# Kernel tuning notes

Measured on AMD Instinct MI355X. Metric: run time of the kernel, lower is better.

The kernel has to match this reference:

```python
import jax, jax.numpy as jnp
import numpy as np

B, T = 1024, 200
V = 100000   # item_size
H = 256      # hidden_size == embedding_size (GRU consumes embedding directly)
NUM_LAYERS = 2


def _gru_layer(x, w_ih, w_hh):
    """PyTorch GRU layer, bias=False. x: [B,T,in], w_ih: [3H,in], w_hh: [3H,H].
    Gate order in weights is (r, z, n)."""
    h0 = jnp.zeros((x.shape[0], w_hh.shape[1]), x.dtype)
    # Precompute all input projections in one big GEMM: [B,T,3H]
    x_proj = jnp.einsum('bti,gi->btg', x, w_ih)

    def step(h, xp):
        hp = h @ w_hh.T                      # [B,3H]
        xr, xz, xn = jnp.split(xp, 3, axis=-1)
        hr, hz, hn = jnp.split(hp, 3, axis=-1)
        r = jax.nn.sigmoid(xr + hr)
        z = jax.nn.sigmoid(xz + hz)
        n = jnp.tanh(xn + r * hn)
        h_new = (1.0 - z) * n + z * h
        return h_new, h_new

    _, ys = jax.lax.scan(step, h0, jnp.swapaxes(x_proj, 0, 1))  # [T,B,H]
    return jnp.swapaxes(ys, 0, 1)  # [B,T,H]


def setup_inputs() -> dict:
    key = jax.random.key(0)
    ks = jax.random.split(key, 8)
    input_ids = jax.random.randint(ks[0], (B, T), 0, V)
    s = 0.05
    emb = jax.random.normal(ks[1], (V, H), jnp.float32) * s
    emb = emb.at[0].set(0.0)  # padding_idx=0
    w_ih_l0 = jax.random.normal(ks[2], (3 * H, H), jnp.float32) * s
    w_hh_l0 = jax.random.normal(ks[3], (3 * H, H), jnp.float32) * s
    w_ih_l1 = jax.random.normal(ks[4], (3 * H, H), jnp.float32) * s
    w_hh_l1 = jax.random.normal(ks[5], (3 * H, H), jnp.float32) * s
    dense_w = jax.random.normal(ks[6], (H, H), jnp.float32) * s  # Linear(H, E=H)
    dense_b = jax.random.normal(ks[7], (H,), jnp.float32) * s
    return {"input_ids": input_ids, "emb": emb,
            "w_ih_l0": w_ih_l0, "w_hh_l0": w_hh_l0,
            "w_ih_l1": w_ih_l1, "w_hh_l1": w_hh_l1,
            "dense_w": dense_w, "dense_b": dense_b}


def reference(input_ids, emb, w_ih_l0, w_hh_l0, w_ih_l1, w_hh_l1, dense_w, dense_b):
    x = emb[input_ids]                 # [B,T,H] embedding lookup
    # emb_dropout is identity in eval mode
    x = _gru_layer(x, w_ih_l0, w_hh_l0)
    x = _gru_layer(x, w_ih_l1, w_hh_l1)
    return x @ dense_w.T + dense_b     # [B,T,H]
```

## Files before the change

kernel.cpp:

```cpp
#include <hip/hip_runtime.h>

#define T_LEN 200
#define HID   256
#define BATCH 1024
#define G3    768
#define ROWS  16
#define NTHREADS 512
#define WSZ   196608

typedef __bf16  bf16x8 __attribute__((ext_vector_type(8)));
typedef float   f32x4  __attribute__((ext_vector_type(4)));

__device__ __forceinline__ unsigned short f2bf(float f) {
  union { float f; unsigned int u; } c; c.f = f;
  unsigned int u = c.u;
  u += 0x7FFFu + ((u >> 16) & 1u);
  return (unsigned short)(u >> 16);
}
__device__ __forceinline__ float bf2f(unsigned int u16v) {
  union { unsigned int u; float f; } c; c.u = u16v << 16; return c.f;
}
__device__ __forceinline__ float sigm(float x) { return 1.0f / (1.0f + __expf(-x)); }
__device__ __forceinline__ float tanh_f(float x) { return 1.0f - 2.0f / (__expf(2.0f * x) + 1.0f); }

__global__ void convert_weights(const float* __restrict__ a,
                                const float* __restrict__ b,
                                const float* __restrict__ c,
                                const float* __restrict__ d,
                                const float* __restrict__ e,
                                unsigned short* __restrict__ out) {
  int i = blockIdx.x * blockDim.x + threadIdx.x;
  const int total = 4 * WSZ + HID * HID;
  if (i >= total) return;
  float v;
  if      (i < 1 * WSZ) v = a[i];
  else if (i < 2 * WSZ) v = b[i - 1 * WSZ];
  else if (i < 3 * WSZ) v = c[i - 2 * WSZ];
  else if (i < 4 * WSZ) v = d[i - 3 * WSZ];
  else                  v = e[i - 4 * WSZ];
  out[i] = f2bf(v);
}

__device__ __forceinline__ bf16x8 lds_frag(const unsigned short* buf, int row, int k, int lq) {
  int chunk = (k << 2) + lq;
  int idx = row * HID + ((chunk ^ (row & 7)) << 3);
  return *reinterpret_cast<const bf16x8*>(buf + idx);
}
__device__ __forceinline__ bf16x8 gw_frag(const unsigned short* __restrict__ W, int wrow, int kof) {
  return *reinterpret_cast<const bf16x8*>(W + (size_t)wrow * HID + kof);
}
__device__ __forceinline__ uint4 gw_fragu(const unsigned short* __restrict__ W, int wrow, int kof) {
  return *reinterpret_cast<const uint4*>(W + (size_t)wrow * HID + kof);
}
__device__ __forceinline__ bf16x8 as_bf(uint4 u) { return __builtin_bit_cast(bf16x8, u); }
__device__ __forceinline__ uint2 pack4(f32x4 v) {
  uint2 r;
  r.x = (unsigned int)f2bf(v[0]) | ((unsigned int)f2bf(v[1]) << 16);
  r.y = (unsigned int)f2bf(v[2]) | ((unsigned int)f2bf(v[3]) << 16);
  return r;
}


template<int GATHER>
__global__ __launch_bounds__(NTHREADS)
void xp_gemm(const int* __restrict__ ids, const float* __restrict__ emb,
             const unsigned short* __restrict__ hsrc,
             const unsigned short* __restrict__ W,
             unsigned short* __restrict__ xpT)
{
  __shared__ __align__(16) unsigned short As[128 * HID];
  const int tid = threadIdx.x;
  const int w = tid >> 6, lane = tid & 63, lr = lane & 15, lq = lane >> 4;
  const int bt = blockIdx.x & 63;
  const int tt = blockIdx.x >> 6;
  const int r0 = bt * 16, t0 = tt * 8;

  for (int idx = tid; idx < 128 * 32; idx += NTHREADS) {
    int row = idx >> 5, cc = idx & 31;
    int bloc = row & 15, tloc = row >> 4;
    int sidx = row * HID + ((cc ^ (row & 7)) << 3);
    if (GATHER) {
      int rid = ids[(r0 + bloc) * T_LEN + t0 + tloc];
      const f32x4* src = reinterpret_cast<const f32x4*>(emb + (size_t)rid * HID + cc * 8);
      f32x4 v0 = src[0], v1 = src[1];
      uint4 pk;
      pk.x = (unsigned int)f2bf(v0[0]) | ((unsigned int)f2bf(v0[1]) << 16);
      pk.y = (unsigned int)f2bf(v0[2]) | ((unsigned int)f2bf(v0[3]) << 16);
      pk.z = (unsigned int)f2bf(v1[0]) | ((unsigned int)f2bf(v1[1]) << 16);
      pk.w = (unsigned int)f2bf(v1[2]) | ((unsigned int)f2bf(v1[3]) << 16);
      *reinterpret_cast<uint4*>(&As[sidx]) = pk;
    } else {
      const unsigned short* hs = hsrc + ((size_t)(t0 + tloc) * 64 + bt) * (ROWS * HID);
      uint4 v = *reinterpret_cast<const uint4*>(hs + bloc * HID + ((cc ^ (bloc & 7)) << 3));
      *reinterpret_cast<uint4*>(&As[sidx]) = v;
    }
  }
  __syncthreads();

  const int colbase = w * 96;
  #pragma unroll 1
  for (int mt = 0; mt < 8; ++mt) {
    bf16x8 a[8];
    #pragma unroll
    for (int k = 0; k < 8; ++k) a[k] = lds_frag(As, mt * 16 + lr, k, lq);
    const int t = t0 + mt;
    unsigned short* xprow = xpT + ((size_t)t * 64 + bt) * (G3 * 16);
    #pragma unroll
    for (int np = 0; np < 3; ++np) {
      const int c0 = colbase + np * 32;
      f32x4 acc0 = {0,0,0,0}, acc1 = {0,0,0,0};
      #pragma unroll
      for (int k = 0; k < 8; ++k) {
        const int kof = k * 32 + lq * 8;
        bf16x8 b0 = gw_frag(W, c0 + lr,      kof);
        bf16x8 b1 = gw_frag(W, c0 + 16 + lr, kof);
        acc0 = __builtin_amdgcn_mfma_f32_16x16x32_bf16(a[k], b0, acc0, 0, 0, 0);
        acc1 = __builtin_amdgcn_mfma_f32_16x16x32_bf16(a[k], b1, acc1, 0, 0, 0);
      }
      *reinterpret_cast<uint2*>(xprow + (c0 + lr)      * 16 + lq * 4) = pack4(acc0);
      *reinterpret_cast<uint2*>(xprow + (c0 + 16 + lr) * 16 + lq * 4) = pack4(acc1);
    }
  }
}

__global__ __launch_bounds__(NTHREADS, 2)
void gru_rec(const unsigned short* __restrict__ xpT,
             const unsigned short* __restrict__ Whh,
             unsigned short* __restrict__ hout)
{
  __shared__ __align__(16) unsigned short hb[2][ROWS * HID];
  const int tid = threadIdx.x;
  const int w = tid >> 6, lane = tid & 63, lr = lane & 15, lq = lane >> 4;
  const int bt = blockIdx.x;
  const int c0 = w * 32;

  uint4 wf[2][3][8];
  #pragma unroll
  for (int j = 0; j < 2; ++j)
    #pragma unroll
    for (int g = 0; g < 3; ++g)
      #pragma unroll
      for (int k = 0; k < 8; ++k)
        wf[j][g][k] = gw_fragu(Whh, g * 256 + c0 + j * 16 + lr, k * 32 + lq * 8);
  #pragma unroll
  for (int j = 0; j < 2; ++j)
    #pragma unroll
    for (int g = 0; g < 3; ++g)
      #pragma unroll
      for (int k = 0; k < 8; ++k)
        asm volatile("" : "+a"(wf[j][g][k].x), "+a"(wf[j][g][k].y),
                          "+a"(wf[j][g][k].z), "+a"(wf[j][g][k].w));

  for (int i = tid; i < ROWS * HID; i += NTHREADS) { hb[0][i] = 0; }

  f32x4 hreg[2] = {{0,0,0,0},{0,0,0,0}};

  const int bj0 = (c0 + lr) * 16 + lq * 4;

  const size_t slabstep = (size_t)64 * G3 * 16;
  const unsigned short* slab = xpT + (size_t)bt * (G3 * 16);
  unsigned short* hslab = hout + (size_t)bt * (ROWS * HID);
  const size_t hstep = (size_t)64 * ROWS * HID;

  __syncthreads();

  uint2 pz[2][3];
  #pragma unroll
  for (int g = 0; g < 3; ++g) {
    pz[0][g] = *reinterpret_cast<const uint2*>(slab + g * 4096 + bj0);
    pz[1][g] = *reinterpret_cast<const uint2*>(slab + g * 4096 + bj0 + 256);
  }

  int cur = 0;
  #pragma unroll 1
  for (int t = 0; t < T_LEN; ++t) {
    f32x4 acc[2][3];
    uint2 xn0 = pz[0][2], xn1 = pz[1][2];
    #pragma unroll
    for (int j = 0; j < 2; ++j) {
      #pragma unroll
      for (int g = 0; g < 2; ++g) {
        uint2 p = pz[j][g];
        f32x4 v;
        v[0] = bf2f(p.x & 0xffffu); v[1] = bf2f(p.x >> 16);
        v[2] = bf2f(p.y & 0xffffu); v[3] = bf2f(p.y >> 16);
        acc[j][g] = v;
      }
      f32x4 z4 = {0,0,0,0};
      acc[j][2] = z4;
    }

    {
      const unsigned short* slab2 = (t + 1 < T_LEN) ? slab + slabstep : slab;
      #pragma unroll
      for (int g = 0; g < 3; ++g) {
        pz[0][g] = *reinterpret_cast<const uint2*>(slab2 + g * 4096 + bj0);
        pz[1][g] = *reinterpret_cast<const uint2*>(slab2 + g * 4096 + bj0 + 256);
      }
    }

    asm volatile("s_waitcnt lgkmcnt(0)\n\ts_barrier" ::: "memory");

    if (t > 0) {
      uint4 hv = *reinterpret_cast<const uint4*>(&hb[cur][tid * 8]);
      *reinterpret_cast<uint4*>(hslab + (size_t)(t - 1) * hstep + tid * 8) = hv;
    }

    #pragma unroll
    for (int k = 0; k < 8; ++k) {
      bf16x8 a = lds_frag(hb[cur], lr, k, lq);
      #pragma unroll
      for (int j = 0; j < 2; ++j) {
        acc[j][0] = __builtin_amdgcn_mfma_f32_16x16x32_bf16(a, as_bf(wf[j][0][k]), acc[j][0], 0, 0, 0);
        acc[j][1] = __builtin_amdgcn_mfma_f32_16x16x32_bf16(a, as_bf(wf[j][1][k]), acc[j][1], 0, 0, 0);
        acc[j][2] = __builtin_amdgcn_mfma_f32_16x16x32_bf16(a, as_bf(wf[j][2][k]), acc[j][2], 0, 0, 0);
      }
    }

    #pragma unroll
    for (int j = 0; j < 2; ++j) {
      uint2 xn = j ? xn1 : xn0;
      float xnv[4];
      xnv[0] = bf2f(xn.x & 0xffffu); xnv[1] = bf2f(xn.x >> 16);
      xnv[2] = bf2f(xn.y & 0xffffu); xnv[3] = bf2f(xn.y >> 16);
      #pragma unroll
      for (int q = 0; q < 4; ++q) {
        float r = sigm(acc[j][0][q]);
        float z = sigm(acc[j][1][q]);
        float n = tanh_f(xnv[q] + r * acc[j][2][q]);
        float hnew = (1.0f - z) * n + z * hreg[j][q];
        hreg[j][q] = hnew;
        int m = lq * 4 + q;
        int c = c0 + j * 16 + lr;
        hb[cur ^ 1][m * HID + (((c >> 3) ^ (m & 7)) << 3) + (c & 7)] = f2bf(hnew);
      }
    }
    slab += slabstep;
    cur ^= 1;
  }

  asm volatile("s_waitcnt lgkmcnt(0)\n\ts_barrier" ::: "memory");
  {
    uint4 hv = *reinterpret_cast<const uint4*>(&hb[cur][tid * 8]);
    *reinterpret_cast<uint4*>(hslab + (size_t)(T_LEN - 1) * hstep + tid * 8) = hv;
  }
}

__global__ __launch_bounds__(NTHREADS)
void dense_gemm(const unsigned short* __restrict__ hsrc,
                const unsigned short* __restrict__ Wd,
                const float* __restrict__ db,
                float* __restrict__ out)
{
  __shared__ __align__(16) unsigned short As[128 * HID];
  const int tid = threadIdx.x;
  const int w = tid >> 6, lane = tid & 63, lr = lane & 15, lq = lane >> 4;
  const int bt = blockIdx.x & 63;
  const int tt = blockIdx.x >> 6;
  const int r0 = bt * 16, t0 = tt * 8;

  for (int idx = tid; idx < 128 * 32; idx += NTHREADS) {
    int row = idx >> 5, cc = idx & 31;
    int bloc = row & 15, tloc = row >> 4;
    int sidx = row * HID + ((cc ^ (row & 7)) << 3);
    const unsigned short* hs = hsrc + ((size_t)(t0 + tloc) * 64 + bt) * (ROWS * HID);
    uint4 v = *reinterpret_cast<const uint4*>(hs + bloc * HID + ((cc ^ (bloc & 7)) << 3));
    *reinterpret_cast<uint4*>(&As[sidx]) = v;
  }
  __syncthreads();

  const int c0 = w * 32;
  const float b0v = db[c0 + lr];
  const float b1v = db[c0 + 16 + lr];

  #pragma unroll 1
  for (int mt = 0; mt < 8; ++mt) {
    bf16x8 a[8];
    #pragma unroll
    for (int k = 0; k < 8; ++k) a[k] = lds_frag(As, mt * 16 + lr, k, lq);
    f32x4 acc0 = {0,0,0,0}, acc1 = {0,0,0,0};
    #pragma unroll
    for (int k = 0; k < 8; ++k) {
      const int kof = k * 32 + lq * 8;
      bf16x8 b0 = gw_frag(Wd, c0 + lr,      kof);
      bf16x8 b1 = gw_frag(Wd, c0 + 16 + lr, kof);
      acc0 = __builtin_amdgcn_mfma_f32_16x16x32_bf16(a[k], b0, acc0, 0, 0, 0);
      acc1 = __builtin_amdgcn_mfma_f32_16x16x32_bf16(a[k], b1, acc1, 0, 0, 0);
    }
    const int t = t0 + mt;
    #pragma unroll
    for (int q = 0; q < 4; ++q) {
      size_t base = ((size_t)(r0 + lq * 4 + q) * T_LEN + t) * HID;
      out[base + c0 + lr]      = acc0[q] + b0v;
      out[base + c0 + 16 + lr] = acc1[q] + b1v;
    }
  }
}

__device__ __forceinline__ void layer_step(
    const bf16x8* ax, const bf16x8* ah,
    const unsigned short* __restrict__ Wih,
    const unsigned short* __restrict__ Whh,
    float (&hreg)[2][4],
    unsigned short* __restrict__ outb,
    int c0base, int lr, int lq)
{
  #pragma unroll
  for (int j = 0; j < 2; ++j) {
    const int c0 = c0base + j * 16;
    f32x4 xr = {0,0,0,0}, xz = {0,0,0,0}, xn = {0,0,0,0};
    f32x4 hr = {0,0,0,0}, hz = {0,0,0,0}, hn = {0,0,0,0};
    #pragma unroll
    for (int k = 0; k < 8; ++k) {
      const int kof = k * 32 + lq * 8;
      bf16x8 b0 = gw_frag(Wih,       c0 + lr, kof);
      bf16x8 b1 = gw_frag(Wih, 256 + c0 + lr, kof);
      bf16x8 b2 = gw_frag(Wih, 512 + c0 + lr, kof);
      bf16x8 w0 = gw_frag(Whh,       c0 + lr, kof);
      bf16x8 w1 = gw_frag(Whh, 256 + c0 + lr, kof);
      bf16x8 w2 = gw_frag(Whh, 512 + c0 + lr, kof);
      xr = __builtin_amdgcn_mfma_f32_16x16x32_bf16(ax[k], b0, xr, 0, 0, 0);
      xz = __builtin_amdgcn_mfma_f32_16x16x32_bf16(ax[k], b1, xz, 0, 0, 0);
      xn = __builtin_amdgcn_mfma_f32_16x16x32_bf16(ax[k], b2, xn, 0, 0, 0);
      hr = __builtin_amdgcn_mfma_f32_16x16x32_bf16(ah[k], w0, hr, 0, 0, 0);
      hz = __builtin_amdgcn_mfma_f32_16x16x32_bf16(ah[k], w1, hz, 0, 0, 0);
      hn = __builtin_amdgcn_mfma_f32_16x16x32_bf16(ah[k], w2, hn, 0, 0, 0);
    }
    #pragma unroll
    for (int q = 0; q < 4; ++q) {
      float r = sigm(xr[q] + hr[q]);
      float z = sigm(xz[q] + hz[q]);
      float n = tanh_f(xn[q] + r * hn[q]);
      float h = (1.0f - z) * n + z * hreg[j][q];
      hreg[j][q] = h;
      int m = lq * 4 + q;
      int c = c0 + lr;
      int idx = m * HID + (((c >> 3) ^ (m & 7)) << 3) + (c & 7);
      outb[idx] = f2bf(h);
    }
  }
}

__global__ __launch_bounds__(NTHREADS)
void gru_fused(const int* __restrict__ ids,
               const float* __restrict__ emb,
               const unsigned short* __restrict__ wbf,
               const float* __restrict__ dense_b,
               float* __restrict__ out)
{
  __shared__ __align__(16) unsigned short x_bf[ROWS * HID];
  __shared__ __align__(16) unsigned short h0b[2][ROWS * HID];
  __shared__ __align__(16) unsigned short h1b[2][ROWS * HID];

  const int tid  = threadIdx.x;
  const int w    = tid >> 6;
  const int lane = tid & 63;
  const int lr   = lane & 15;
  const int lq   = lane >> 4;
  const int r0   = blockIdx.x * ROWS;
  const int c0base = w * 32;

  const unsigned short* Wih0 = wbf;
  const unsigned short* Whh0 = wbf + 1 * WSZ;
  const unsigned short* Wih1 = wbf + 2 * WSZ;
  const unsigned short* Whh1 = wbf + 3 * WSZ;
  const unsigned short* Wd   = wbf + 4 * WSZ;

  for (int i = tid; i < ROWS * HID; i += NTHREADS) {
    h0b[0][i] = 0; h0b[1][i] = 0; h1b[0][i] = 0; h1b[1][i] = 0;
  }
  float hreg0[2][4] = {}; float hreg1[2][4] = {};
  const float bias0 = dense_b[c0base + lr];
  const float bias1 = dense_b[c0base + 16 + lr];

  const int grow   = tid >> 5;
  const int gchunk = tid & 31;
  const int gswz   = grow * HID + ((gchunk ^ (grow & 7)) << 3);
  const int gid_base = (r0 + grow) * T_LEN;

  __syncthreads();

  int cur = 0;
  for (int t = 0; t < T_LEN; ++t) {
    {
      int rid = ids[gid_base + t];
      const f32x4* src = reinterpret_cast<const f32x4*>(emb + (size_t)rid * HID + gchunk * 8);
      f32x4 v0 = src[0];
      f32x4 v1 = src[1];
      uint4 pk;
      pk.x = (unsigned int)f2bf(v0[0]) | ((unsigned int)f2bf(v0[1]) << 16);
      pk.y = (unsigned int)f2bf(v0[2]) | ((unsigned int)f2bf(v0[3]) << 16);
      pk.z = (unsigned int)f2bf(v1[0]) | ((unsigned int)f2bf(v1[1]) << 16);
      pk.w = (unsigned int)f2bf(v1[2]) | ((unsigned int)f2bf(v1[3]) << 16);
      *reinterpret_cast<uint4*>(&x_bf[gswz]) = pk;
    }
    __syncthreads();

    bf16x8 ax[8], ah[8];
    #pragma unroll
    for (int k = 0; k < 8; ++k) {
      ax[k] = lds_frag(x_bf,     lr, k, lq);
      ah[k] = lds_frag(h0b[cur], lr, k, lq);
    }
    layer_step(ax, ah, Wih0, Whh0, hreg0, h0b[cur ^ 1], c0base, lr, lq);
    __syncthreads();

    #pragma unroll
    for (int k = 0; k < 8; ++k) {
      ax[k] = lds_frag(h0b[cur ^ 1], lr, k, lq);
      ah[k] = lds_frag(h1b[cur],     lr, k, lq);
    }
    layer_step(ax, ah, Wih1, Whh1, hreg1, h1b[cur ^ 1], c0base, lr, lq);
    __syncthreads();

    #pragma unroll
    for (int k = 0; k < 8; ++k) ax[k] = lds_frag(h1b[cur ^ 1], lr, k, lq);
    #pragma unroll
    for (int j = 0; j < 2; ++j) {
      const int c0 = c0base + j * 16;
      f32x4 acc = {0,0,0,0};
      #pragma unroll
      for (int k = 0; k < 8; ++k) {
        bf16x8 bw = gw_frag(Wd, c0 + lr, k * 32 + lq * 8);
        acc = __builtin_amdgcn_mfma_f32_16x16x32_bf16(ax[k], bw, acc, 0, 0, 0);
      }
      const float bias = j ? bias1 : bias0;
      size_t base = ((size_t)(r0 + lq * 4) * T_LEN + t) * HID + c0 + lr;
      #pragma unroll
      for (int q = 0; q < 4; ++q) {
        out[base + (size_t)q * T_LEN * HID] = acc[q] + bias;
      }
    }
    cur ^= 1;
  }
}

extern "C" void kernel_launch(void* const* d_in, const int* in_sizes, int n_in,
                              void* d_out, int out_size, void* d_ws, size_t ws_size,
                              hipStream_t stream) {
  const int*   ids  = (const int*)d_in[0];
  const float* emb  = (const float*)d_in[1];
  const float* wih0 = (const float*)d_in[2];
  const float* whh0 = (const float*)d_in[3];
  const float* wih1 = (const float*)d_in[4];
  const float* whh1 = (const float*)d_in[5];
  const float* dw   = (const float*)d_in[6];
  const float* db   = (const float*)d_in[7];

  unsigned short* wbf = (unsigned short*)d_ws;

  const int total = 4 * WSZ + HID * HID;
  convert_weights<<<(total + 255) / 256, 256, 0, stream>>>(wih0, whh0, wih1, whh1, dw, wbf);

  const size_t XP_OFF = 2u * 1024u * 1024u;
  const size_t XP_BYTES = (size_t)T_LEN * G3 * BATCH * 2;
  const size_t H_OFF  = XP_OFF + XP_BYTES;
  const size_t H_BYTES = (size_t)BATCH * T_LEN * HID * 2;
  const size_t NEED = H_OFF + H_BYTES;

  if (ws_size >= NEED) {
    unsigned short* xpT  = (unsigned short*)((char*)d_ws + XP_OFF);
    unsigned short* hbuf = (unsigned short*)((char*)d_ws + H_OFF);
    const unsigned short* Wih0 = wbf;
    const unsigned short* Whh0 = wbf + 1 * WSZ;
    const unsigned short* Wih1 = wbf + 2 * WSZ;
    const unsigned short* Whh1 = wbf + 3 * WSZ;
    const unsigned short* Wd   = wbf + 4 * WSZ;

    xp_gemm<1><<<1600, NTHREADS, 0, stream>>>(ids, emb, nullptr, Wih0, xpT);
    gru_rec<<<64, NTHREADS, 0, stream>>>(xpT, Whh0, hbuf);
    xp_gemm<0><<<1600, NTHREADS, 0, stream>>>(nullptr, nullptr, hbuf, Wih1, xpT);
    gru_rec<<<64, NTHREADS, 0, stream>>>(xpT, Whh1, hbuf);
    dense_gemm<<<1600, NTHREADS, 0, stream>>>(hbuf, Wd, db, (float*)d_out);
  } else {
    gru_fused<<<64, NTHREADS, 0, stream>>>(ids, emb, wbf, db, (float*)d_out);
  }
}
```

Before: 2.382 ms.

## Split GRU recurrence across 128 blocks of 8 rows and fuse dense into layer-1

After: 4.195 ms. +76.1%, slower.

```diff
diff --git a/kernel.cpp b/kernel.cpp
--- a/kernel.cpp
+++ b/kernel.cpp
@@ -5,6 +5,8 @@
 #define BATCH 1024
 #define G3    768
 #define ROWS  16
+#define RROWS 8
+#define NBLK  128
 #define NTHREADS 512
 #define WSZ   196608
 
@@ -104,7 +106,8 @@
     #pragma unroll
     for (int k = 0; k < 8; ++k) a[k] = lds_frag(As, mt * 16 + lr, k, lq);
     const int t = t0 + mt;
-    unsigned short* xprow = xpT + ((size_t)t * 64 + bt) * (G3 * 16);
+    unsigned short* xprow = xpT + ((size_t)t * NBLK + (r0 >> 3) + (lq >> 1)) * (G3 * RROWS)
+                                + (lq & 1) * 4;
     #pragma unroll
     for (int np = 0; np < 3; ++np) {
       const int c0 = colbase + np * 32;
@@ -117,21 +120,21 @@
         acc0 = __builtin_amdgcn_mfma_f32_16x16x32_bf16(a[k], b0, acc0, 0, 0, 0);
         acc1 = __builtin_amdgcn_mfma_f32_16x16x32_bf16(a[k], b1, acc1, 0, 0, 0);
       }
-      *reinterpret_cast<uint2*>(xprow + (c0 + lr)      * 16 + lq * 4) = pack4(acc0);
-      *reinterpret_cast<uint2*>(xprow + (c0 + 16 + lr) * 16 + lq * 4) = pack4(acc1);
+      *reinterpret_cast<uint2*>(xprow + (c0 + lr)      * RROWS) = pack4(acc0);
+      *reinterpret_cast<uint2*>(xprow + (c0 + 16 + lr) * RROWS) = pack4(acc1);
     }
   }
 }
 
 __global__ __launch_bounds__(NTHREADS, 2)
-void gru_rec(const unsigned short* __restrict__ xpT,
-             const unsigned short* __restrict__ Whh,
-             unsigned short* __restrict__ hout)
+void gru_rec0(const unsigned short* __restrict__ xpT,
+              const unsigned short* __restrict__ Whh,
+              unsigned short* __restrict__ hout)
 {
   __shared__ __align__(16) unsigned short hb[2][ROWS * HID];
   const int tid = threadIdx.x;
   const int w = tid >> 6, lane = tid & 63, lr = lane & 15, lq = lane >> 4;
-  const int bt = blockIdx.x;
+  const int b = blockIdx.x;
   const int c0 = w * 32;
 
   uint4 wf[2][3][8];
@@ -151,24 +154,25 @@
         asm volatile("" : "+a"(wf[j][g][k].x), "+a"(wf[j][g][k].y),
                           "+a"(wf[j][g][k].z), "+a"(wf[j][g][k].w));
 
-  for (int i = tid; i < ROWS * HID; i += NTHREADS) { hb[0][i] = 0; }
+  for (int i = tid; i < ROWS * HID; i += NTHREADS) { hb[0][i] = 0; hb[1][i] = 0; }
 
   f32x4 hreg[2] = {{0,0,0,0},{0,0,0,0}};
 
-  const int bj0 = (c0 + lr) * 16 + lq * 4;
-
-  const size_t slabstep = (size_t)64 * G3 * 16;
-  const unsigned short* slab = xpT + (size_t)bt * (G3 * 16);
-  unsigned short* hslab = hout + (size_t)bt * (ROWS * HID);
-  const size_t hstep = (size_t)64 * ROWS * HID;
+  const int rowoff = (lq & 1) * 4;
+  const int bj0 = (c0 + lr) * RROWS + rowoff;
+
+  const size_t slabstep = (size_t)NBLK * G3 * RROWS;
+  const unsigned short* slab = xpT + (size_t)b * (G3 * RROWS);
+  unsigned short* hslab = hout + (size_t)(b >> 1) * (ROWS * HID) + (size_t)(b & 1) * (RROWS * HID);
+  const size_t hstep = (size_t)64 * (ROWS * HID);
 
   __syncthreads();
 
   uint2 pz[2][3];
   #pragma unroll
   for (int g = 0; g < 3; ++g) {
-    pz[0][g] = *reinterpret_cast<const uint2*>(slab + g * 4096 + bj0);
-    pz[1][g] = *reinterpret_cast<const uint2*>(slab + g * 4096 + bj0 + 256);
+    pz[0][g] = *reinterpret_cast<const uint2*>(slab + g * 2048 + bj0);
+    pz[1][g] = *reinterpret_cast<const uint2*>(slab + g * 2048 + bj0 + 128);
   }
 
   int cur = 0;
@@ -194,14 +198,14 @@
       const unsigned short* slab2 = (t + 1 < T_LEN) ? slab + slabstep : slab;
       #pragma unroll
       for (int g = 0; g < 3; ++g) {
-        pz[0][g] = *reinterpret_cast<const uint2*>(slab2 + g * 4096 + bj0);
-        pz[1][g] = *reinterpret_cast<const uint2*>(slab2 + g * 4096 + bj0 + 256);
+        pz[0][g] = *reinterpret_cast<const uint2*>(slab2 + g * 2048 + bj0);
+        pz[1][g] = *reinterpret_cast<const uint2*>(slab2 + g * 2048 + bj0 + 128);
       }
     }
 
     asm volatile("s_waitcnt lgkmcnt(0)\n\ts_barrier" ::: "memory");
 
-    if (t > 0) {
+    if (t > 0 && tid < 256) {
       uint4 hv = *reinterpret_cast<const uint4*>(&hb[cur][tid * 8]);
       *reinterpret_cast<uint4*>(hslab + (size_t)(t - 1) * hstep + tid * 8) = hv;
     }
@@ -228,11 +232,13 @@
         float r = sigm(acc[j][0][q]);
         float z = sigm(acc[j][1][q]);
         float n = tanh_f(xnv[q] + r * acc[j][2][q]);
-        float hnew = (1.0f - z) * n + z * hreg[j][q];
+        float hnew = fmaf(z, hreg[j][q] - n, n);
         hreg[j][q] = hnew;
-        int m = lq * 4 + q;
-        int c = c0 + j * 16 + lr;
-        hb[cur ^ 1][m * HID + (((c >> 3) ^ (m & 7)) << 3) + (c & 7)] = f2bf(hnew);
+        if (lq < 2) {
+          int m = lq * 4 + q;
+          int c = c0 + j * 16 + lr;
+          hb[cur ^ 1][m * HID + (((c >> 3) ^ (m & 7)) << 3) + (c & 7)] = f2bf(hnew);
+        }
       }
     }
     slab += slabstep;
@@ -240,59 +246,179 @@
   }
 
   asm volatile("s_waitcnt lgkmcnt(0)\n\ts_barrier" ::: "memory");
-  {
+  if (tid < 256) {
     uint4 hv = *reinterpret_cast<const uint4*>(&hb[cur][tid * 8]);
     *reinterpret_cast<uint4*>(hslab + (size_t)(T_LEN - 1) * hstep + tid * 8) = hv;
   }
 }
 
-__global__ __launch_bounds__(NTHREADS)
-void dense_gemm(const unsigned short* __restrict__ hsrc,
-                const unsigned short* __restrict__ Wd,
-                const float* __restrict__ db,
-                float* __restrict__ out)
+__global__ __launch_bounds__(NTHREADS, 2)
+void gru_rec1(const unsigned short* __restrict__ xpT,
+              const unsigned short* __restrict__ Whh,
+              const unsigned short* __restrict__ Wd,
+              const float* __restrict__ db,
+              float* __restrict__ out)
 {
-  __shared__ __align__(16) unsigned short As[128 * HID];
+  __shared__ __align__(16) unsigned short hb[2][ROWS * HID];
   const int tid = threadIdx.x;
   const int w = tid >> 6, lane = tid & 63, lr = lane & 15, lq = lane >> 4;
-  const int bt = blockIdx.x & 63;
-  const int tt = blockIdx.x >> 6;
-  const int r0 = bt * 16, t0 = tt * 8;
-
-  for (int idx = tid; idx < 128 * 32; idx += NTHREADS) {
-    int row = idx >> 5, cc = idx & 31;
-    int bloc = row & 15, tloc = row >> 4;
-    int sidx = row * HID + ((cc ^ (row & 7)) << 3);
-    const unsigned short* hs = hsrc + ((size_t)(t0 + tloc) * 64 + bt) * (ROWS * HID);
-    uint4 v = *reinterpret_cast<const uint4*>(hs + bloc * HID + ((cc ^ (bloc & 7)) << 3));
-    *reinterpret_cast<uint4*>(&As[sidx]) = v;
-  }
-  __syncthreads();
-
+  const int b = blockIdx.x;
+  const int r0 = b * RROWS;
   const int c0 = w * 32;
+
+  uint4 wf[2][3][8];
+  #pragma unroll
+  for (int j = 0; j < 2; ++j)
+    #pragma unroll
+    for (int g = 0; g < 3; ++g)
+      #pragma unroll
+      for (int k = 0; k < 8; ++k)
+        wf[j][g][k] = gw_fragu(Whh, g * 256 + c0 + j * 16 + lr, k * 32 + lq * 8);
+  uint4 wfd[2][8];
+  #pragma unroll
+  for (int j = 0; j < 2; ++j)
+    #pragma unroll
+    for (int k = 0; k < 8; ++k)
+      wfd[j][k] = gw_fragu(Wd, c0 + j * 16 + lr, k * 32 + lq * 8);
+  #pragma unroll
+  for (int j = 0; j < 2; ++j)
+    #pragma unroll
+    for (int g = 0; g < 3; ++g)
+      #pragma unroll
+      for (int k = 0; k < 8; ++k)
+        asm volatile("" : "+a"(wf[j][g][k].x), "+a"(wf[j][g][k].y),
+                          "+a"(wf[j][g][k].z), "+a"(wf[j][g][k].w));
+  #pragma unroll
+  for (int j = 0; j < 2; ++j)
+    #pragma unroll
+    for (int k = 0; k < 8; ++k)
+      asm volatile("" : "+a"(wfd[j][k].x), "+a"(wfd[j][k].y),
+                        "+a"(wfd[j][k].z), "+a"(wfd[j][k].w));
+
+  for (int i = tid; i < ROWS * HID; i += NTHREADS) { hb[0][i] = 0; hb[1][i] = 0; }
+
+  f32x4 hreg[2] = {{0,0,0,0},{0,0,0,0}};
   const float b0v = db[c0 + lr];
   const float b1v = db[c0 + 16 + lr];
 
+  const int rowoff = (lq & 1) * 4;
+  const int bj0 = (c0 + lr) * RROWS + rowoff;
+
+  const size_t slabstep = (size_t)NBLK * G3 * RROWS;
+  const unsigned short* slab = xpT + (size_t)b * (G3 * RROWS);
+
+  __syncthreads();
+
+  uint2 pz[2][3];
+  #pragma unroll
+  for (int g = 0; g < 3; ++g) {
+    pz[0][g] = *reinterpret_cast<const uint2*>(slab + g * 2048 + bj0);
+    pz[1][g] = *reinterpret_cast<const uint2*>(slab + g * 2048 + bj0 + 128);
+  }
+
+  int cur = 0;
   #pragma unroll 1
-  for (int mt = 0; mt < 8; ++mt) {
+  for (int t = 0; t < T_LEN; ++t) {
+    f32x4 acc[2][3];
+    uint2 xn0 = pz[0][2], xn1 = pz[1][2];
+    #pragma unroll
+    for (int j = 0; j < 2; ++j) {
+      #pragma unroll
+      for (int g = 0; g < 2; ++g) {
+        uint2 p = pz[j][g];
+        f32x4 v;
+        v[0] = bf2f(p.x & 0xffffu); v[1] = bf2f(p.x >> 16);
+        v[2] = bf2f(p.y & 0xffffu); v[3] = bf2f(p.y >> 16);
+        acc[j][g] = v;
+      }
+      f32x4 z4 = {0,0,0,0};
+      acc[j][2] = z4;
+    }
+
+    {
+      const unsigned short* slab2 = (t + 1 < T_LEN) ? slab + slabstep : slab;
+      #pragma unroll
+      for (int g = 0; g < 3; ++g) {
+        pz[0][g] = *reinterpret_cast<const uint2*>(slab2 + g * 2048 + bj0);
+        pz[1][g] = *reinterpret_cast<const uint2*>(slab2 + g * 2048 + bj0 + 128);
+      }
+    }
+
+    asm volatile("s_waitcnt lgkmcnt(0)\n\ts_barrier" ::: "memory");
+
     bf16x8 a[8];
     #pragma unroll
-    for (int k = 0; k < 8; ++k) a[k] = lds_frag(As, mt * 16 + lr, k, lq);
-    f32x4 acc0 = {0,0,0,0}, acc1 = {0,0,0,0};
+    for (int k = 0; k < 8; ++k) a[k] = lds_frag(hb[cur], lr, k, lq);
+
+    if (t > 0) {
+      f32x4 d0 = {0,0,0,0}, d1 = {0,0,0,0};
+      #pragma unroll
+      for (int k = 0; k < 8; ++k) {
+        d0 = __builtin_amdgcn_mfma_f32_16x16x32_bf16(a[k], as_bf(wfd[0][k]), d0, 0, 0, 0);
+        d1 = __builtin_amdgcn_mfma_f32_16x16x32_bf16(a[k], as_bf(wfd[1][k]), d1, 0, 0, 0);
+      }
+      if (lq < 2) {
+        #pragma unroll
+        for (int q = 0; q < 4; ++q) {
+          size_t base = ((size_t)(r0 + lq * 4 + q) * T_LEN + (t - 1)) * HID;
+          out[base + c0 + lr]      = d0[q] + b0v;
+          out[base + c0 + 16 + lr] = d1[q] + b1v;
+        }
+      }
+    }
+
     #pragma unroll
     for (int k = 0; k < 8; ++k) {
-      const int kof = k * 32 + lq * 8;
-      bf16x8 b0 = gw_frag(Wd, c0 + lr,      kof);
-      bf16x8 b1 = gw_frag(Wd, c0 + 16 + lr, kof);
-      acc0 = __builtin_amdgcn_mfma_f32_16x16x32_bf16(a[k], b0, acc0, 0, 0, 0);
-      acc1 = __builtin_amdgcn_mfma_f32_16x16x32_bf16(a[k], b1, acc1, 0, 0, 0);
-    }
-    const int t = t0 + mt;
-    #pragma unroll
-    for (int q = 0; q < 4; ++q) {
-      size_t base = ((size_t)(r0 + lq * 4 + q) * T_LEN + t) * HID;
-      out[base + c0 + lr]      = acc0[q] + b0v;
-      out[base + c0 + 16 + lr] = acc1[q] + b1v;
+      #pragma unroll
+      for (int j = 0; j < 2; ++j) {
+        acc[j][0] = __builtin_amdgcn_mfma_f32_16x16x32_bf16(a[k], as_bf(wf[j][0][k]), acc[j][0], 0, 0, 0);
+        acc[j][1] = __builtin_amdgcn_mfma_f32_16x16x32_bf16(a[k], as_bf(wf[j][1][k]), acc[j][1], 0, 0, 0);
+        acc[j][2] = __builtin_amdgcn_mfma_f32_16x16x32_bf16(a[k], as_bf(wf[j][2][k]), acc[j][2], 0, 0, 0);
+      }
+    }
+
+    #pragma unroll
+    for (int j = 0; j < 2; ++j) {
+      uint2 xn = j ? xn1 : xn0;
+      float xnv[4];
+      xnv[0] = bf2f(xn.x & 0xffffu); xnv[1] = bf2f(xn.x >> 16);
+      xnv[2] = bf2f(xn.y & 0xffffu); xnv[3] = bf2f(xn.y >> 16);
+      #pragma unroll
+      for (int q = 0; q < 4; ++q) {
+        float r = sigm(acc[j][0][q]);
+        float z = sigm(acc[j][1][q]);
+        float n = tanh_f(xnv[q] + r * acc[j][2][q]);
+        float hnew = fmaf(z, hreg[j][q] - n, n);
+        hreg[j][q] = hnew;
+        if (lq < 2) {
+          int m = lq * 4 + q;
+          int c = c0 + j * 16 + lr;
+          hb[cur ^ 1][m * HID + (((c >> 3) ^ (m & 7)) << 3) + (c & 7)] = f2bf(hnew);
+        }
+      }
+    }
+    slab += slabstep;
+    cur ^= 1;
+  }
+
+  asm volatile("s_waitcnt lgkmcnt(0)\n\ts_barrier" ::: "memory");
+  {
+    bf16x8 a[8];
+    #pragma unroll
+    for (int k = 0; k < 8; ++k) a[k] = lds_frag(hb[cur], lr, k, lq);
+    f32x4 d0 = {0,0,0,0}, d1 = {0,0,0,0};
+    #pragma unroll
+    for (int k = 0; k < 8; ++k) {
+      d0 = __builtin_amdgcn_mfma_f32_16x16x32_bf16(a[k], as_bf(wfd[0][k]), d0, 0, 0, 0);
+      d1 = __builtin_amdgcn_mfma_f32_16x16x32_bf16(a[k], as_bf(wfd[1][k]), d1, 0, 0, 0);
+    }
+    if (lq < 2) {
+      #pragma unroll
+      for (int q = 0; q < 4; ++q) {
+        size_t base = ((size_t)(r0 + lq * 4 + q) * T_LEN + (T_LEN - 1)) * HID;
+        out[base + c0 + lr]      = d0[q] + b0v;
+        out[base + c0 + 16 + lr] = d1[q] + b1v;
+      }
     }
   }
 }
@@ -468,10 +594,9 @@
     const unsigned short* Wd   = wbf + 4 * WSZ;
 
     xp_gemm<1><<<1600, NTHREADS, 0, stream>>>(ids, emb, nullptr, Wih0, xpT);
-    gru_rec<<<64, NTHREADS, 0, stream>>>(xpT, Whh0, hbuf);
+    gru_rec0<<<NBLK, NTHREADS, 0, stream>>>(xpT, Whh0, hbuf);
     xp_gemm<0><<<1600, NTHREADS, 0, stream>>>(nullptr, nullptr, hbuf, Wih1, xpT);
-    gru_rec<<<64, NTHREADS, 0, stream>>>(xpT, Whh1, hbuf);
-    dense_gemm<<<1600, NTHREADS, 0, stream>>>(hbuf, Wd, db, (float*)d_out);
+    gru_rec1<<<NBLK, NTHREADS, 0, stream>>>(xpT, Whh1, Wd, db, (float*)d_out);
   } else {
     gru_fused<<<64, NTHREADS, 0, stream>>>(ids, emb, wbf, db, (float*)d_out);
   }
```
